# Kernel optimization log

Measured on AMD Instinct MI355X. Metric: run time of the kernel, lower is better.

## Reference

```python
import jax, jax.numpy as jnp
import numpy as np

E = 64       # expert_nums
D = 32       # embed_dim
H = 4        # num_heads
HD = D // H  # head_dim = 8
B = 524288
TOP_K = 2
NOISE_EPS = 0.01


def setup_inputs() -> dict:
    key = jax.random.key(0)
    ks = jax.random.split(key, 10)
    return {
        "taskID": jax.random.randint(ks[0], (B,), 0, 6),
        "embed_table": jax.random.normal(ks[1], (6, D), jnp.float32),
        "expert_keys": jax.random.normal(ks[2], (D, D), jnp.float32),
        "in_proj_w": jax.random.normal(ks[3], (3 * D, D), jnp.float32) * 0.1,
        "in_proj_b": jax.random.normal(ks[4], (3 * D,), jnp.float32) * 0.1,
        "fc_gate_w": jax.random.normal(ks[5], (E, D), jnp.float32) * 0.1,
        "fc_gate_b": jax.random.normal(ks[6], (E,), jnp.float32) * 0.1,
        "fc_noise_w": jax.random.normal(ks[7], (E, D), jnp.float32) * 0.1,
        "fc_noise_b": jax.random.normal(ks[8], (E,), jnp.float32) * 0.1,
        "noise": jax.random.normal(ks[9], (B, E), jnp.float32),
    }


def reference(taskID, embed_table, expert_keys, in_proj_w, in_proj_b,
              fc_gate_w, fc_gate_b, fc_noise_w, fc_noise_b, noise):
    bsz = taskID.shape[0]
    x = embed_table[taskID]                                   # [B, D] task embeddings (query)
    # nn.MultiheadAttention q/k projections (v and out_proj don't affect attn_weights)
    Wq, Wk = in_proj_w[:D], in_proj_w[D:2 * D]
    bq, bk = in_proj_b[:D], in_proj_b[D:2 * D]
    Q = (x @ Wq.T + bq).reshape(bsz, H, HD)                   # [B, H, HD]
    K = (expert_keys @ Wk.T + bk).reshape(D, H, HD)           # [S=32, H, HD], shared across batch
    scores = jnp.einsum('bhd,shd->bhs', Q, K) / np.sqrt(HD).astype(np.float32)
    attn_w = jax.nn.softmax(scores, axis=-1).mean(axis=1)     # averaged over heads -> [B, 32]
    expert_weight = jax.nn.softmax(attn_w, axis=-1)           # module re-applies softmax (faithful)
    clean_logits = expert_weight @ fc_gate_w.T + fc_gate_b    # [B, E]
    noise_std = jax.nn.softplus(expert_weight @ fc_noise_w.T + fc_noise_b) + NOISE_EPS
    logits = clean_logits + noise * noise_std                 # train=True path
    top_logits, top_indices = jax.lax.top_k(logits, min(TOP_K + 1, E))
    tk_logits = top_logits[:, :TOP_K]                         # [B, TOP_K]
    tk_indices = top_indices[:, :TOP_K]
    tk_gates = jax.nn.softmax(tk_logits, axis=-1)
    rows = jnp.arange(bsz)[:, None]
    gates = jnp.zeros_like(logits).at[rows, tk_indices].set(tk_gates)  # scatter sparse gates
    load = gates.sum(axis=0)                                  # [E]
    return gates, load
```

## Files before the change

### kernel.cpp

```cpp
#include <hip/hip_runtime.h>
#include <math.h>

#define NE 64
#define NTASK 6
#define BLK 256
#define GRID 1024
#define RPI 32

__global__ void precompute_kernel(
    const float* __restrict__ embed_table,
    const float* __restrict__ expert_keys,
    const float* __restrict__ in_proj_w,
    const float* __restrict__ in_proj_b,
    const float* __restrict__ fc_gate_w,
    const float* __restrict__ fc_gate_b,
    const float* __restrict__ fc_noise_w,
    const float* __restrict__ fc_noise_b,
    float*   __restrict__ tab_f,
    double2* __restrict__ tab_d,
    float*   __restrict__ load)
{
    __shared__ float s_win[96 * 32];
    __shared__ float s_wg[64 * 32];
    __shared__ float s_wn[64 * 32];
    __shared__ float s_keys[32 * 32];
    __shared__ float s_emb[6 * 32];
    __shared__ float s_bin[96], s_bg[64], s_bn[64];
    __shared__ double Ksh[32][32];
    __shared__ double Qsh[6][32];
    __shared__ double sc[24][32];
    __shared__ double attn[6][32];
    __shared__ double ew[6][32];
    __shared__ double red[24];
    __shared__ double red2[6];
    const int tid = threadIdx.x;

    if (tid < NE) load[tid] = 0.f;

    for (int i = tid; i < 96 * 32; i += BLK) s_win[i] = in_proj_w[i];
    for (int i = tid; i < 64 * 32; i += BLK) { s_wg[i] = fc_gate_w[i]; s_wn[i] = fc_noise_w[i]; }
    for (int i = tid; i < 32 * 32; i += BLK) s_keys[i] = expert_keys[i];
    for (int i = tid; i < 6 * 32;  i += BLK) s_emb[i] = embed_table[i];
    if (tid < 96) s_bin[tid] = in_proj_b[tid];
    if (tid < 64) { s_bg[tid] = fc_gate_b[tid]; s_bn[tid] = fc_noise_b[tid]; }
    __syncthreads();

    for (int idx = tid; idx < 32 * 32; idx += BLK) {
        int s = idx >> 5, j = idx & 31;
        double acc = (double)s_bin[32 + j];
        for (int d = 0; d < 32; ++d)
            acc += (double)s_keys[s * 32 + d] * (double)s_win[(32 + j) * 32 + d];
        Ksh[s][j] = acc;
    }
    for (int idx = tid; idx < NTASK * 32; idx += BLK) {
        int t = idx >> 5, j = idx & 31;
        double acc = (double)s_bin[j];
        for (int d = 0; d < 32; ++d)
            acc += (double)s_emb[t * 32 + d] * (double)s_win[j * 32 + d];
        Qsh[t][j] = acc;
    }
    __syncthreads();

    const double SCALE = 1.0 / (double)((float)2.8284271247461903);
    for (int idx = tid; idx < 24 * 32; idx += BLK) {
        int th = idx >> 5, s = idx & 31;
        int t = th >> 2, h = th & 3;
        double acc = 0.0;
        for (int d = 0; d < 8; ++d)
            acc += Qsh[t][h * 8 + d] * Ksh[s][h * 8 + d];
        sc[th][s] = acc * SCALE;
    }
    __syncthreads();
    if (tid < 24) {
        double m = sc[tid][0];
        for (int s = 1; s < 32; ++s) m = fmax(m, sc[tid][s]);
        red[tid] = m;
    }
    __syncthreads();
    for (int idx = tid; idx < 24 * 32; idx += BLK) {
        int th = idx >> 5, s = idx & 31;
        sc[th][s] = exp(sc[th][s] - red[th]);
    }
    __syncthreads();
    if (tid < 24) {
        double sum = 0.0;
        for (int s = 0; s < 32; ++s) sum += sc[tid][s];
        red[tid] = 1.0 / sum;
    }
    __syncthreads();
    for (int idx = tid; idx < NTASK * 32; idx += BLK) {
        int t = idx >> 5, s = idx & 31;
        attn[t][s] = 0.25 * (sc[t*4+0][s]*red[t*4+0] + sc[t*4+1][s]*red[t*4+1]
                           + sc[t*4+2][s]*red[t*4+2] + sc[t*4+3][s]*red[t*4+3]);
    }
    __syncthreads();
    if (tid < NTASK) {
        double m = attn[tid][0];
        for (int s = 1; s < 32; ++s) m = fmax(m, attn[tid][s]);
        red2[tid] = m;
    }
    __syncthreads();
    for (int idx = tid; idx < NTASK * 32; idx += BLK) {
        int t = idx >> 5, s = idx & 31;
        ew[t][s] = exp(attn[t][s] - red2[t]);
    }
    __syncthreads();
    if (tid < NTASK) {
        double sum = 0.0;
        for (int s = 0; s < 32; ++s) sum += ew[tid][s];
        red2[tid] = 1.0 / sum;
    }
    __syncthreads();

    {
        float2* tab_f2 = (float2*)tab_f;
        for (int idx = tid; idx < NTASK * NE; idx += BLK) {
            int t = idx >> 6, e = idx & 63;
            double inv = red2[t];
            double a  = (double)s_bg[e];
            double n0 = (double)s_bn[e];
            for (int d = 0; d < 32; ++d) {
                double w = ew[t][d] * inv;
                a  += w * (double)s_wg[e * 32 + d];
                n0 += w * (double)s_wn[e * 32 + d];
            }
            double sp = (n0 > 0.0) ? (n0 + log1p(exp(-n0))) : log1p(exp(n0));
            double ns = sp + 0.01;
            const int p  = e >> 1;
            const int cc = (p >> 3) & 3, rr = p & 7;
            const int i4 = t * 32 + p;
            const int dst = (i4 & ~7) | (rr ^ ((2 * cc + t) & 7));
            tab_f2[dst * 2 + (e & 1)] = make_float2((float)a, (float)ns);
            tab_d[t * 64 + e] = make_double2(a, ns);
        }
        for (int idx = NTASK * NE + tid; idx < 512; idx += BLK) {
            tab_f2[idx] = make_float2(0.f, 0.f);
        }
    }
}

__global__ __launch_bounds__(BLK) void router_kernel(
    const int*     __restrict__ taskID,
    const float4*  __restrict__ noise4,
    const float4*  __restrict__ tabf4,
    const double2* __restrict__ tabd,
    float4* __restrict__ gates4,
    float*  __restrict__ load,
    int B)
{
    __shared__ float4  s_tabf4[256];
    __shared__ double2 s_tabd[512];
    __shared__ float   s_load[NE];
    __shared__ float4  s_stage[BLK/64][256];

    const int tid = threadIdx.x;
    for (int i = tid; i < 256; i += BLK) s_tabf4[i] = tabf4[i];
    for (int i = tid; i < 512; i += BLK) s_tabd[i] = tabd[i];
    if (tid < NE) s_load[tid] = 0.f;
    __syncthreads();

    const int lane  = tid & 63;
    const int wid   = tid >> 6;
    const int sub   = lane >> 2;
    const int c     = lane & 3;
    const int ebase = c * 16;
    const int W = (blockIdx.x * BLK + tid) >> 6;
    const int nWaves = GRID * (BLK / 64);
    const int nGroup = (B + RPI - 1) / RPI;
    const int n4 = B * 16;
    const float4 zero4 = make_float4(0.f, 0.f, 0.f, 0.f);

    float4 cur[8], nxt[8];
    int tA = 0, tB = 0;

    {
        const int gb = W * 512;
        #pragma unroll
        for (int j = 0; j < 8; ++j) {
            const int idx = gb + j * 64 + lane;
            cur[j] = (W < nGroup && idx < n4) ? noise4[idx] : zero4;
        }
        const int rA = W * RPI + sub, rB = rA + 16;
        tA = (W < nGroup && rA < B) ? taskID[rA] : 0;
        tB = (W < nGroup && rB < B) ? taskID[rB] : 0;
    }

    for (int g = W; g < nGroup; g += nWaves) {
        const int gn = g + nWaves;
        {
            const int gb = gn * 512;
            #pragma unroll
            for (int j = 0; j < 8; ++j) {
                const int idx = gb + j * 64 + lane;
                nxt[j] = (gn < nGroup && idx < n4) ? noise4[idx] : zero4;
            }
        }
        int ntA = 0, ntB = 0;
        {
            const int rA = gn * RPI + sub, rB = rA + 16;
            ntA = (gn < nGroup && rA < B) ? taskID[rA] : 0;
            ntB = (gn < nGroup && rB < B) ? taskID[rB] : 0;
        }

#define INS2(l_, e_, n_) {                                                     \
        const bool b1_ = (l_) > v1, b2_ = (l_) > v2;                           \
        v2 = b1_ ? v1 : (b2_ ? (l_) : v2);                                     \
        i2 = b1_ ? i1 : (b2_ ? (e_) : i2);                                     \
        n2 = b1_ ? n1 : (b2_ ? (n_) : n2);                                     \
        v1 = b1_ ? (l_) : v1;                                                  \
        i1 = b1_ ? (e_) : i1;                                                  \
        n1 = b1_ ? (n_) : n1; }

#define STEP(r_, nlo_, nhi_) {                                                 \
        const float4 tv = s_tabf4[tb + ((r_) ^ x)];                            \
        const float l0 = __fadd_rn(tv.x, __fmul_rn((nlo_), tv.y));             \
        const float l1 = __fadd_rn(tv.z, __fmul_rn((nhi_), tv.w));             \
        INS2(l0, ebase + 2 * (r_),     (nlo_));                                \
        INS2(l1, ebase + 2 * (r_) + 1, (nhi_)); }

#define PROCHALF(t_, rowbase_, cj0, cj1, cj2, cj3)                             \
    {                                                                          \
                         \
        _Pragma("unroll")                                                      \
        for (int j = 0; j < 4; ++j) {                                          \
            const float4 vsrc = (j == 0) ? (cj0) : (j == 1) ? (cj1)            \
                              : (j == 2) ? (cj2) : (cj3);                      \
            const int f  = j * 64 + lane;                                      \
            const int rl = f >> 4, q = f & 15;                                 \
            s_stage[wid][rl * 16 + (q ^ rl)] = vsrc;                           \
        }                                                                      \
        float4 z[4];                                                           \
        _Pragma("unroll")                                                      \
        for (int k = 0; k < 4; ++k)                                            \
            z[k] = s_stage[wid][sub * 16 + ((c * 4 + k) ^ sub)];               \
        const int t  = (t_);                                                   \
        const int x  = (2 * c + t) & 7;                                        \
        const int tb = t * 32 + c * 8;                                         \
        float v1 = -INFINITY, v2 = -INFINITY;                                  \
        int   i1 = 0, i2 = 0;                                                  \
        float n1 = 0.f, n2 = 0.f;                                              \
        STEP(0, z[0].x, z[0].y); STEP(1, z[0].z, z[0].w);                      \
        STEP(2, z[1].x, z[1].y); STEP(3, z[1].z, z[1].w);                      \
        STEP(4, z[2].x, z[2].y); STEP(5, z[2].z, z[2].w);                      \
        STEP(6, z[3].x, z[3].y); STEP(7, z[3].z, z[3].w);                      \
        _Pragma("unroll")                                                      \
        for (int m = 1; m <= 2; m <<= 1) {                                     \
            const float w1 = __shfl_xor(v1, m), w2 = __shfl_xor(v2, m);        \
            const int   j1 = __shfl_xor(i1, m), j2 = __shfl_xor(i2, m);        \
            const float q1 = __shfl_xor(n1, m), q2 = __shfl_xor(n2, m);        \
            const bool aw = (v1 > w1) || (v1 == w1 && i1 < j1);                \
            const float p1 = aw ? v1 : w1, p2 = aw ? v2 : w2;                  \
            const int   pi1 = aw ? i1 : j1, pi2 = aw ? i2 : j2;                \
            const float pn1 = aw ? n1 : q1, pn2 = aw ? n2 : q2;                \
            const float u1 = aw ? w1 : v1;                                     \
            const int   ui1 = aw ? j1 : i1;                                    \
            const float un1 = aw ? q1 : n1;                                    \
            const bool b2 = (p2 > u1) || (p2 == u1 && pi2 < ui1);              \
            v1 = p1;  i1 = pi1; n1 = pn1;                                      \
            v2 = b2 ? p2 : u1;  i2 = b2 ? pi2 : ui1;  n2 = b2 ? pn2 : un1;     \
        }                                                                      \
        const double2 A  = s_tabd[t * 64 + i1];                                \
        const double2 Bt = s_tabd[t * 64 + i2];                                \
        double da = A.x  + (double)n1 * A.y;  int ia = i1;                     \
        double db = Bt.x + (double)n2 * Bt.y; int ib = i2;                     \
        if (db > da || (db == da && ib < ia)) {                                \
            double tv_ = da; da = db; db = tv_;                                \
            int ti_ = ia; ia = ib; ib = ti_;                                   \
        }                                                                      \
        const float e2 = expf((float)(db - da));                               \
        const float g1 = 1.0f / (1.0f + e2);                                   \
        const float g2 = e2 / (1.0f + e2);                                     \
        const int iab = ia | (ib << 8);                                        \
        if (c == 0 && ((rowbase_) + sub) < B) {                                \
            atomicAdd(&s_load[ia], g1);                                        \
            atomicAdd(&s_load[ib], g2);                                        \
        }                                                                      \
         \
        const int gb_ = (rowbase_) * 16;                                       \
        _Pragma("unroll")                                                      \
        for (int j = 0; j < 4; ++j) {                                          \
            const int f  = j * 64 + lane;                                      \
            const int rr = f >> 4;                                             \
            const int p  = f & 15;                                             \
            const int src = rr << 2;                                           \
            const int   siab = __shfl(iab, src);                               \
            const float sg1  = __shfl(g1,  src);                               \
            const float sg2  = __shfl(g2,  src);                               \
            const int sia = siab & 255, sib = siab >> 8;                       \
            const int e0 = p * 4;                                              \
            float4 w;                                                          \
            w.x = (e0 + 0 == sia) ? sg1 : ((e0 + 0 == sib) ? sg2 : 0.f);       \
            w.y = (e0 + 1 == sia) ? sg1 : ((e0 + 1 == sib) ? sg2 : 0.f);       \
            w.z = (e0 + 2 == sia) ? sg1 : ((e0 + 2 == sib) ? sg2 : 0.f);       \
            w.w = (e0 + 3 == sia) ? sg1 : ((e0 + 3 == sib) ? sg2 : 0.f);       \
            const int gidx = gb_ + f;                                          \
            if (gidx < n4) gates4[gidx] = w;                                   \
        }                                                                      \
    }

        PROCHALF(tA, g * RPI,      cur[0], cur[1], cur[2], cur[3])
        PROCHALF(tB, g * RPI + 16, cur[4], cur[5], cur[6], cur[7])

#undef PROCHALF
#undef STEP
#undef INS2

        #pragma unroll
        for (int j = 0; j < 8; ++j) cur[j] = nxt[j];
        tA = ntA; tB = ntB;
    }
    __syncthreads();
    if (tid < NE) atomicAdd(&load[tid], s_load[tid]);
}

extern "C" void kernel_launch(void* const* d_in, const int* in_sizes, int n_in,
                              void* d_out, int out_size, void* d_ws, size_t ws_size,
                              hipStream_t stream) {
    const int*   taskID      = (const int*)  d_in[0];
    const float* embed_table = (const float*)d_in[1];
    const float* expert_keys = (const float*)d_in[2];
    const float* in_proj_w   = (const float*)d_in[3];
    const float* in_proj_b   = (const float*)d_in[4];
    const float* fc_gate_w   = (const float*)d_in[5];
    const float* fc_gate_b   = (const float*)d_in[6];
    const float* fc_noise_w  = (const float*)d_in[7];
    const float* fc_noise_b  = (const float*)d_in[8];
    const float* noise       = (const float*)d_in[9];

    const int B = in_sizes[0];

    float*   tab_f = (float*)d_ws;
    double2* tab_d = (double2*)((char*)d_ws + 4096);

    float* gates = (float*)d_out;
    float* load  = gates + (size_t)B * NE;

    precompute_kernel<<<1, BLK, 0, stream>>>(embed_table, expert_keys, in_proj_w, in_proj_b,
                                             fc_gate_w, fc_gate_b, fc_noise_w, fc_noise_b,
                                             tab_f, tab_d, load);

    router_kernel<<<GRID, BLK, 0, stream>>>(taskID, (const float4*)noise,
                                            (const float4*)tab_f, tab_d,
                                            (float4*)gates, load, B);
}
```

Before: 119.6 us.

## Drop double-precision top-2 recheck, split top-2 scan into two chains, raise grid

Removes the double-precision table and the refinement that recomputed the two winning logits in fp64 and reordered them. Gates now come straight from the float top-2 values. The per-thread top-2 insertion is split into two independent chains that are merged at the end, which shortens the serial dependency. The grid grows from 1024 to 1280 blocks. This cuts shared memory and fp64 work per row, at the risk of different tie and rounding behaviour when two logits are nearly equal.

After: 115.1 us. -3.8%, faster.

```diff
diff --git a/kernel.cpp b/kernel.cpp
--- a/kernel.cpp
+++ b/kernel.cpp
@@ -4,7 +4,7 @@
 #define NE 64
 #define NTASK 6
 #define BLK 256
-#define GRID 1024
+#define GRID 1280
 #define RPI 32
 
 __global__ void precompute_kernel(
@@ -17,7 +17,6 @@
     const float* __restrict__ fc_noise_w,
     const float* __restrict__ fc_noise_b,
     float*   __restrict__ tab_f,
-    double2* __restrict__ tab_d,
     float*   __restrict__ load)
 {
     __shared__ float s_win[96 * 32];
@@ -131,7 +130,6 @@
             const int i4 = t * 32 + p;
             const int dst = (i4 & ~7) | (rr ^ ((2 * cc + t) & 7));
             tab_f2[dst * 2 + (e & 1)] = make_float2((float)a, (float)ns);
-            tab_d[t * 64 + e] = make_double2(a, ns);
         }
         for (int idx = NTASK * NE + tid; idx < 512; idx += BLK) {
             tab_f2[idx] = make_float2(0.f, 0.f);
@@ -143,19 +141,16 @@
     const int*     __restrict__ taskID,
     const float4*  __restrict__ noise4,
     const float4*  __restrict__ tabf4,
-    const double2* __restrict__ tabd,
     float4* __restrict__ gates4,
     float*  __restrict__ load,
     int B)
 {
-    __shared__ float4  s_tabf4[256];
-    __shared__ double2 s_tabd[512];
-    __shared__ float   s_load[NE];
-    __shared__ float4  s_stage[BLK/64][256];
+    __shared__ float4 s_tabf4[256];
+    __shared__ float  s_load[NE];
+    __shared__ float4 s_stage[BLK/64][256];
 
     const int tid = threadIdx.x;
     for (int i = tid; i < 256; i += BLK) s_tabf4[i] = tabf4[i];
-    for (int i = tid; i < 512; i += BLK) s_tabd[i] = tabd[i];
     if (tid < NE) s_load[tid] = 0.f;
     __syncthreads();
 
@@ -202,25 +197,24 @@
             ntB = (gn < nGroup && rB < B) ? taskID[rB] : 0;
         }
 
-#define INS2(l_, e_, n_) {                                                     \
-        const bool b1_ = (l_) > v1, b2_ = (l_) > v2;                           \
-        v2 = b1_ ? v1 : (b2_ ? (l_) : v2);                                     \
-        i2 = b1_ ? i1 : (b2_ ? (e_) : i2);                                     \
-        n2 = b1_ ? n1 : (b2_ ? (n_) : n2);                                     \
-        v1 = b1_ ? (l_) : v1;                                                  \
-        i1 = b1_ ? (e_) : i1;                                                  \
-        n1 = b1_ ? (n_) : n1; }
-
-#define STEP(r_, nlo_, nhi_) {                                                 \
+#define INS2C(V1,I1,N1,V2,I2,N2, l_, e_, n_) {                                 \
+        const bool b1_ = (l_) > V1, b2_ = (l_) > V2;                           \
+        V2 = b1_ ? V1 : (b2_ ? (l_) : V2);                                     \
+        I2 = b1_ ? I1 : (b2_ ? (e_) : I2);                                     \
+        N2 = b1_ ? N1 : (b2_ ? (n_) : N2);                                     \
+        V1 = b1_ ? (l_) : V1;                                                  \
+        I1 = b1_ ? (e_) : I1;                                                  \
+        N1 = b1_ ? (n_) : N1; }
+
+#define STEPC(V1,I1,N1,V2,I2,N2, r_, nlo_, nhi_) {                             \
         const float4 tv = s_tabf4[tb + ((r_) ^ x)];                            \
         const float l0 = __fadd_rn(tv.x, __fmul_rn((nlo_), tv.y));             \
         const float l1 = __fadd_rn(tv.z, __fmul_rn((nhi_), tv.w));             \
-        INS2(l0, ebase + 2 * (r_),     (nlo_));                                \
-        INS2(l1, ebase + 2 * (r_) + 1, (nhi_)); }
+        INS2C(V1,I1,N1,V2,I2,N2, l0, ebase + 2 * (r_),     (nlo_));            \
+        INS2C(V1,I1,N1,V2,I2,N2, l1, ebase + 2 * (r_) + 1, (nhi_)); }
 
 #define PROCHALF(t_, rowbase_, cj0, cj1, cj2, cj3)                             \
     {                                                                          \
-                         \
         _Pragma("unroll")                                                      \
         for (int j = 0; j < 4; ++j) {                                          \
             const float4 vsrc = (j == 0) ? (cj0) : (j == 1) ? (cj1)            \
@@ -236,13 +230,30 @@
         const int t  = (t_);                                                   \
         const int x  = (2 * c + t) & 7;                                        \
         const int tb = t * 32 + c * 8;                                         \
-        float v1 = -INFINITY, v2 = -INFINITY;                                  \
-        int   i1 = 0, i2 = 0;                                                  \
-        float n1 = 0.f, n2 = 0.f;                                              \
-        STEP(0, z[0].x, z[0].y); STEP(1, z[0].z, z[0].w);                      \
-        STEP(2, z[1].x, z[1].y); STEP(3, z[1].z, z[1].w);                      \
-        STEP(4, z[2].x, z[2].y); STEP(5, z[2].z, z[2].w);                      \
-        STEP(6, z[3].x, z[3].y); STEP(7, z[3].z, z[3].w);                      \
+                  \
+        float vA1 = -INFINITY, vA2 = -INFINITY, vB1 = -INFINITY, vB2 = -INFINITY; \
+        int   iA1 = 0, iA2 = 0, iB1 = 0, iB2 = 0;                              \
+        float nA1 = 0.f, nA2 = 0.f, nB1 = 0.f, nB2 = 0.f;                      \
+        STEPC(vA1,iA1,nA1,vA2,iA2,nA2, 0, z[0].x, z[0].y);                     \
+        STEPC(vB1,iB1,nB1,vB2,iB2,nB2, 4, z[2].x, z[2].y);                     \
+        STEPC(vA1,iA1,nA1,vA2,iA2,nA2, 1, z[0].z, z[0].w);                     \
+        STEPC(vB1,iB1,nB1,vB2,iB2,nB2, 5, z[2].z, z[2].w);                     \
+        STEPC(vA1,iA1,nA1,vA2,iA2,nA2, 2, z[1].x, z[1].y);                     \
+        STEPC(vB1,iB1,nB1,vB2,iB2,nB2, 6, z[3].x, z[3].y);                     \
+        STEPC(vA1,iA1,nA1,vA2,iA2,nA2, 3, z[1].z, z[1].w);                     \
+        STEPC(vB1,iB1,nB1,vB2,iB2,nB2, 7, z[3].z, z[3].w);                     \
+                  \
+        float v1, v2, n1, n2; int i1, i2;                                      \
+        if (vB1 > vA1) {                                                       \
+            v1 = vB1; i1 = iB1; n1 = nB1;                                      \
+            const bool s2 = vB2 > vA1;                                         \
+            v2 = s2 ? vB2 : vA1; i2 = s2 ? iB2 : iA1; n2 = s2 ? nB2 : nA1;     \
+        } else {                                                               \
+            v1 = vA1; i1 = iA1; n1 = nA1;                                      \
+            const bool s2 = vB1 > vA2;                                         \
+            v2 = s2 ? vB1 : vA2; i2 = s2 ? iB1 : iA2; n2 = s2 ? nB1 : nA2;     \
+        }                                                                      \
+                           \
         _Pragma("unroll")                                                      \
         for (int m = 1; m <= 2; m <<= 1) {                                     \
             const float w1 = __shfl_xor(v1, m), w2 = __shfl_xor(v2, m);        \
@@ -259,23 +270,16 @@
             v1 = p1;  i1 = pi1; n1 = pn1;                                      \
             v2 = b2 ? p2 : u1;  i2 = b2 ? pi2 : ui1;  n2 = b2 ? pn2 : un1;     \
         }                                                                      \
-        const double2 A  = s_tabd[t * 64 + i1];                                \
-        const double2 Bt = s_tabd[t * 64 + i2];                                \
-        double da = A.x  + (double)n1 * A.y;  int ia = i1;                     \
-        double db = Bt.x + (double)n2 * Bt.y; int ib = i2;                     \
-        if (db > da || (db == da && ib < ia)) {                                \
-            double tv_ = da; da = db; db = tv_;                                \
-            int ti_ = ia; ia = ib; ib = ti_;                                   \
-        }                                                                      \
-        const float e2 = expf((float)(db - da));                               \
+                              \
+        const float e2 = expf(v2 - v1);                                        \
         const float g1 = 1.0f / (1.0f + e2);                                   \
         const float g2 = e2 / (1.0f + e2);                                     \
+        const int ia = i1, ib = i2;                                            \
         const int iab = ia | (ib << 8);                                        \
         if (c == 0 && ((rowbase_) + sub) < B) {                                \
             atomicAdd(&s_load[ia], g1);                                        \
             atomicAdd(&s_load[ib], g2);                                        \
         }                                                                      \
-         \
         const int gb_ = (rowbase_) * 16;                                       \
         _Pragma("unroll")                                                      \
         for (int j = 0; j < 4; ++j) {                                          \
@@ -302,8 +306,8 @@
         PROCHALF(tB, g * RPI + 16, cur[4], cur[5], cur[6], cur[7])
 
 #undef PROCHALF
-#undef STEP
-#undef INS2
+#undef STEPC
+#undef INS2C
 
         #pragma unroll
         for (int j = 0; j < 8; ++j) cur[j] = nxt[j];
@@ -329,17 +333,16 @@
 
     const int B = in_sizes[0];
 
-    float*   tab_f = (float*)d_ws;
-    double2* tab_d = (double2*)((char*)d_ws + 4096);
+    float* tab_f = (float*)d_ws;
 
     float* gates = (float*)d_out;
     float* load  = gates + (size_t)B * NE;
 
     precompute_kernel<<<1, BLK, 0, stream>>>(embed_table, expert_keys, in_proj_w, in_proj_b,
                                              fc_gate_w, fc_gate_b, fc_noise_w, fc_noise_b,
-                                             tab_f, tab_d, load);
+                                             tab_f, load);
 
     router_kernel<<<GRID, BLK, 0, stream>>>(taskID, (const float4*)noise,
-                                            (const float4*)tab_f, tab_d,
+                                            (const float4*)tab_f,
                                             (float4*)gates, load, B);
 }
```
